# Performance work log

Hardware: AMD Instinct MI355X
Metric: run time of the kernel (lower is better)

The kernel has to match this reference:

```python
import jax, jax.numpy as jnp
import numpy as np

B, C, NX, NY = 4, 64, 432, 496
G = NX * NY
P_PER = 20000


def setup_inputs() -> dict:
    key = jax.random.key(0)
    ks = jax.random.split(key, 4)
    rng = np.random.default_rng(0)
    coords = []
    for b in range(B):
        flat = rng.choice(G, P_PER, replace=False)  # unique BEV cells per batch
        y, x = flat // NX, flat % NX
        coords.append(np.stack([np.full(P_PER, b), np.zeros(P_PER, np.int64), y, x], 1))
    coords = jnp.asarray(np.concatenate(coords, 0), dtype=jnp.int32)  # [P,4] = (b,z,y,x)
    return {
        "pillar_features": jax.random.normal(ks[0], (B * P_PER, C), jnp.float32),
        "W_off": jax.random.normal(ks[1], (2, C), jnp.float32) * 0.05,
        "b_off": jnp.zeros((2,), jnp.float32),
        "W_step": jax.random.normal(ks[2], (1, C), jnp.float32) * 0.05,
        "b_step": jnp.zeros((1,), jnp.float32),
        "W_prob": jax.random.normal(ks[3], (1, C), jnp.float32) * 0.05,
        "b_prob": jnp.zeros((1,), jnp.float32),
        "voxel_coords": coords,
    }


def reference(pillar_features, W_off, b_off, W_step, b_step, W_prob, b_prob, voxel_coords):
    # flat scatter index per pillar: batch*G + (z + y*nx + x), nz==1 so z==0
    b_idx = voxel_coords[:, 0].astype(jnp.int32)
    idx = voxel_coords[:, 1] + voxel_coords[:, 2] * NX + voxel_coords[:, 3]
    gidx = b_idx * G + idx  # [P]

    # dense BEV scatter (indices are unique per batch -> set semantics match torch)
    spatial = jnp.zeros((B * G, C), pillar_features.dtype).at[gidx].set(pillar_features)

    # VotingModule heads on pillar features
    offset = jnp.tanh(pillar_features @ W_off.T + b_off)          # [P,2]
    step = jax.nn.relu(pillar_features @ W_step.T + b_step)       # [P,1]
    prob = jax.nn.sigmoid(pillar_features @ W_prob.T + b_prob)    # [P,1]

    cent = jnp.zeros((B * G, 2), pillar_features.dtype).at[gidx].set(offset)
    # NOTE: original code writes step then immediately overwrites with prob (bug kept)
    step_buf = jnp.zeros((B * G, 1), pillar_features.dtype).at[gidx].set(prob)
    prob_buf = jnp.zeros((B * G, 1), pillar_features.dtype)  # never written (bug kept)

    # get_propagatated_feature: shift features by offset*step, weighted by prob
    off_y = cent[:, 0] * step_buf[:, 0]
    off_x = cent[:, 1] * step_buf[:, 0]
    yy = jnp.tile(jnp.repeat(jnp.arange(NY), NX), B).astype(jnp.float32)
    xx = jnp.tile(jnp.tile(jnp.arange(NX), NY), B).astype(jnp.float32)
    ty = jnp.clip(jnp.round(yy + off_y), 0, NY - 1).astype(jnp.int32)
    tx = jnp.clip(jnp.round(xx + off_x), 0, NX - 1).astype(jnp.int32)
    bb = jnp.repeat(jnp.arange(B, dtype=jnp.int32), G)
    tgt = bb * G + ty * NX + tx  # [B*G]

    p = prob_buf  # [B*G,1]
    out = jnp.zeros((B * G, C), spatial.dtype).at[tgt].add(spatial * p) + spatial * (1.0 - p)
    return out.reshape(B, NY, NX, C).transpose(0, 3, 1, 2)  # [B,C,ny,nx]
```

## Files before the change

kernel.cpp:

```cpp
#include <hip/hip_runtime.h>
#include <hip/hip_bf16.h>

#define BB 4
#define CC 64
#define NXX 432
#define NYY 496
#define GG (NXX * NYY)
#define PP 80000

typedef float v4f __attribute__((ext_vector_type(4)));


#define ZROW_INT_OFF (BB * GG)

__global__ void k_init_map(int* __restrict__ map) {
    int i = blockIdx.x * blockDim.x + threadIdx.x;
    const int n4 = (BB * GG) / 4;
    if (i < n4) {
        ((int4*)map)[i] = make_int4(-1, -1, -1, -1);
    }
    if (i < 16) {
        ((int4*)(map + ZROW_INT_OFF))[i] = make_int4(0, 0, 0, 0);
    }
}

__global__ void k_scatter_ids(const int* __restrict__ coords, int* __restrict__ map) {
    int i = blockIdx.x * blockDim.x + threadIdx.x;
    if (i < PP) {
        int4 cd = ((const int4*)coords)[i];
        int g = cd.x * GG + cd.y + cd.z * NXX + cd.w;
        map[g] = i;
    }
}

__global__ void __launch_bounds__(256, 4) k_gather(const float* __restrict__ pf,
                                                   const int* __restrict__ map,
                                                   float* __restrict__ out) {
    int t = blockIdx.x * blockDim.x + threadIdx.x;
    const int nGroups = (BB * GG) / 4;
    if (t >= nGroups) return;

    int cellBase = t * 4;
    int b = cellBase / GG;
    int cellInB = cellBase - b * GG;

    int4 pids = ((const int4*)map)[t];
    const v4f* pf4 = (const v4f*)pf;
    const v4f* z4  = (const v4f*)(map + ZROW_INT_OFF);

    const v4f* p0 = (pids.x >= 0) ? (pf4 + pids.x * 16) : z4;
    const v4f* p1 = (pids.y >= 0) ? (pf4 + pids.y * 16) : z4;
    const v4f* p2 = (pids.z >= 0) ? (pf4 + pids.z * 16) : z4;
    const v4f* p3 = (pids.w >= 0) ? (pf4 + pids.w * 16) : z4;

    float* outBase = out + (size_t)(b * CC) * GG + cellInB;

    #pragma unroll
    for (int g = 0; g < 4; ++g) {
        v4f r[4][4];
        #pragma unroll
        for (int j = 0; j < 4; ++j) {
            r[j][0] = p0[g * 4 + j];
            r[j][1] = p1[g * 4 + j];
            r[j][2] = p2[g * 4 + j];
            r[j][3] = p3[g * 4 + j];
        }
        #pragma unroll
        for (int j = 0; j < 4; ++j) {
            int c0 = (g * 4 + j) * 4;
            v4f w0 = (v4f){r[j][0].x, r[j][1].x, r[j][2].x, r[j][3].x};
            v4f w1 = (v4f){r[j][0].y, r[j][1].y, r[j][2].y, r[j][3].y};
            v4f w2 = (v4f){r[j][0].z, r[j][1].z, r[j][2].z, r[j][3].z};
            v4f w3 = (v4f){r[j][0].w, r[j][1].w, r[j][2].w, r[j][3].w};

            *(v4f*)(outBase + (size_t)(c0 + 0) * GG) = w0;
            *(v4f*)(outBase + (size_t)(c0 + 1) * GG) = w1;
            *(v4f*)(outBase + (size_t)(c0 + 2) * GG) = w2;
            *(v4f*)(outBase + (size_t)(c0 + 3) * GG) = w3;
        }
    }
}

extern "C" void kernel_launch(void* const* d_in, const int* in_sizes, int n_in,
                              void* d_out, int out_size, void* d_ws, size_t ws_size,
                              hipStream_t stream) {
    const float* pf     = (const float*)d_in[0];
    const int*   coords = (const int*)d_in[7];
    float*       out    = (float*)d_out;
    int*         map    = (int*)d_ws;

    const int n4 = (BB * GG) / 4;
    k_init_map<<<dim3((n4 + 255) / 256), dim3(256), 0, stream>>>(map);
    k_scatter_ids<<<dim3((PP + 255) / 256), dim3(256), 0, stream>>>(coords, map);

    const int nGroups = (BB * GG) / 4;
    k_gather<<<dim3((nGroups + 255) / 256), dim3(256), 0, stream>>>(pf, map, out);
}
```

Before: 252.2 us.

## Fuse init, scatter and gather into one cooperative persistent kernel

Replaces three kernel launches with a single cooperative kernel that uses grid-wide syncs between the map init, pillar-id scatter and dense gather phases, with grid-stride loops over a persistent grid sized from occupancy (assuming 256 CUs). This removes launch overhead and inter-kernel gaps. In exchange it adds grid.sync costs, and the persistent grid may give less latency hiding for the bandwidth-bound gather than a full oversubscribed grid.

Result: slower. 391.3 us (+55.1%).

```diff
diff --git a/kernel.cpp b/kernel.cpp
--- a/kernel.cpp
+++ b/kernel.cpp
@@ -1,5 +1,7 @@
 #include <hip/hip_runtime.h>
-#include <hip/hip_bf16.h>
+#include <hip/hip_cooperative_groups.h>
+
+namespace cg = cooperative_groups;
 
 #define BB 4
 #define CC 64
@@ -13,70 +15,68 @@
 
 #define ZROW_INT_OFF (BB * GG)
 
-__global__ void k_init_map(int* __restrict__ map) {
-    int i = blockIdx.x * blockDim.x + threadIdx.x;
+__global__ void __launch_bounds__(256, 4) k_fused(const float* __restrict__ pf,
+                                                  const int* __restrict__ coords,
+                                                  int* __restrict__ map,
+                                                  float* __restrict__ out) {
+    cg::grid_group grid = cg::this_grid();
+    const int tid = blockIdx.x * blockDim.x + threadIdx.x;
+    const int nthr = gridDim.x * blockDim.x;
     const int n4 = (BB * GG) / 4;
-    if (i < n4) {
+
+    for (int i = tid; i < n4; i += nthr)
         ((int4*)map)[i] = make_int4(-1, -1, -1, -1);
+    if (tid < 16)
+        ((int4*)(map + ZROW_INT_OFF))[tid] = make_int4(0, 0, 0, 0);
+
+    grid.sync();
+
+    for (int i = tid; i < PP; i += nthr) {
+        int4 cd = ((const int4*)coords)[i];
+        map[cd.x * GG + cd.y + cd.z * NXX + cd.w] = i;
     }
-    if (i < 16) {
-        ((int4*)(map + ZROW_INT_OFF))[i] = make_int4(0, 0, 0, 0);
-    }
-}
 
-__global__ void k_scatter_ids(const int* __restrict__ coords, int* __restrict__ map) {
-    int i = blockIdx.x * blockDim.x + threadIdx.x;
-    if (i < PP) {
-        int4 cd = ((const int4*)coords)[i];
-        int g = cd.x * GG + cd.y + cd.z * NXX + cd.w;
-        map[g] = i;
-    }
-}
+    grid.sync();
 
-__global__ void __launch_bounds__(256, 4) k_gather(const float* __restrict__ pf,
-                                                   const int* __restrict__ map,
-                                                   float* __restrict__ out) {
-    int t = blockIdx.x * blockDim.x + threadIdx.x;
-    const int nGroups = (BB * GG) / 4;
-    if (t >= nGroups) return;
-
-    int cellBase = t * 4;
-    int b = cellBase / GG;
-    int cellInB = cellBase - b * GG;
-
-    int4 pids = ((const int4*)map)[t];
     const v4f* pf4 = (const v4f*)pf;
     const v4f* z4  = (const v4f*)(map + ZROW_INT_OFF);
 
-    const v4f* p0 = (pids.x >= 0) ? (pf4 + pids.x * 16) : z4;
-    const v4f* p1 = (pids.y >= 0) ? (pf4 + pids.y * 16) : z4;
-    const v4f* p2 = (pids.z >= 0) ? (pf4 + pids.z * 16) : z4;
-    const v4f* p3 = (pids.w >= 0) ? (pf4 + pids.w * 16) : z4;
+    for (int t = tid; t < n4; t += nthr) {
+        int cellBase = t * 4;
+        int b = cellBase / GG;
+        int cellInB = cellBase - b * GG;
 
-    float* outBase = out + (size_t)(b * CC) * GG + cellInB;
+        int4 pids = ((const int4*)map)[t];
+        const v4f* p0 = (pids.x >= 0) ? (pf4 + pids.x * 16) : z4;
+        const v4f* p1 = (pids.y >= 0) ? (pf4 + pids.y * 16) : z4;
+        const v4f* p2 = (pids.z >= 0) ? (pf4 + pids.z * 16) : z4;
+        const v4f* p3 = (pids.w >= 0) ? (pf4 + pids.w * 16) : z4;
 
-    #pragma unroll
-    for (int g = 0; g < 4; ++g) {
-        v4f r[4][4];
+        float* outBase = out + (size_t)(b * CC) * GG + cellInB;
+
         #pragma unroll
-        for (int j = 0; j < 4; ++j) {
-            r[j][0] = p0[g * 4 + j];
-            r[j][1] = p1[g * 4 + j];
-            r[j][2] = p2[g * 4 + j];
-            r[j][3] = p3[g * 4 + j];
-        }
-        #pragma unroll
-        for (int j = 0; j < 4; ++j) {
-            int c0 = (g * 4 + j) * 4;
-            v4f w0 = (v4f){r[j][0].x, r[j][1].x, r[j][2].x, r[j][3].x};
-            v4f w1 = (v4f){r[j][0].y, r[j][1].y, r[j][2].y, r[j][3].y};
-            v4f w2 = (v4f){r[j][0].z, r[j][1].z, r[j][2].z, r[j][3].z};
-            v4f w3 = (v4f){r[j][0].w, r[j][1].w, r[j][2].w, r[j][3].w};
+        for (int g = 0; g < 4; ++g) {
+            v4f r[4][4];
+            #pragma unroll
+            for (int j = 0; j < 4; ++j) {
+                r[j][0] = p0[g * 4 + j];
+                r[j][1] = p1[g * 4 + j];
+                r[j][2] = p2[g * 4 + j];
+                r[j][3] = p3[g * 4 + j];
+            }
+            #pragma unroll
+            for (int j = 0; j < 4; ++j) {
+                int c0 = (g * 4 + j) * 4;
+                v4f w0 = (v4f){r[j][0].x, r[j][1].x, r[j][2].x, r[j][3].x};
+                v4f w1 = (v4f){r[j][0].y, r[j][1].y, r[j][2].y, r[j][3].y};
+                v4f w2 = (v4f){r[j][0].z, r[j][1].z, r[j][2].z, r[j][3].z};
+                v4f w3 = (v4f){r[j][0].w, r[j][1].w, r[j][2].w, r[j][3].w};
 
-            *(v4f*)(outBase + (size_t)(c0 + 0) * GG) = w0;
-            *(v4f*)(outBase + (size_t)(c0 + 1) * GG) = w1;
-            *(v4f*)(outBase + (size_t)(c0 + 2) * GG) = w2;
-            *(v4f*)(outBase + (size_t)(c0 + 3) * GG) = w3;
+                *(v4f*)(outBase + (size_t)(c0 + 0) * GG) = w0;
+                *(v4f*)(outBase + (size_t)(c0 + 1) * GG) = w1;
+                *(v4f*)(outBase + (size_t)(c0 + 2) * GG) = w2;
+                *(v4f*)(outBase + (size_t)(c0 + 3) * GG) = w3;
+            }
         }
     }
 }
@@ -89,10 +89,16 @@
     float*       out    = (float*)d_out;
     int*         map    = (int*)d_ws;
 
-    const int n4 = (BB * GG) / 4;
-    k_init_map<<<dim3((n4 + 255) / 256), dim3(256), 0, stream>>>(map);
-    k_scatter_ids<<<dim3((PP + 255) / 256), dim3(256), 0, stream>>>(coords, map);
+    static int nBlocks = 0;
+    if (nBlocks == 0) {
+        int nb = 0;
+        hipError_t e = hipOccupancyMaxActiveBlocksPerMultiprocessor(&nb, k_fused, 256, 0);
+        if (e != hipSuccess || nb < 1) nb = 2;
+        if (nb > 8) nb = 8;
+        nBlocks = nb * 256;
+    }
 
-    const int nGroups = (BB * GG) / 4;
-    k_gather<<<dim3((nGroups + 255) / 256), dim3(256), 0, stream>>>(pf, map, out);
+    void* args[] = {(void*)&pf, (void*)&coords, (void*)&map, (void*)&out};
+    hipLaunchCooperativeKernel((const void*)k_fused, dim3(nBlocks), dim3(256),
+                               args, 0, stream);
 }
```
